# Kernel tuning notes

Hardware: AMD Instinct MI355X
Metric: run time of the kernel (lower is better)

## Reference

```python
import jax, jax.numpy as jnp
import numpy as np

N_WIRES = 4
DIM = 2 ** N_WIRES  # 16 amplitudes per 4-qubit state
# PauliZ sign table: wire 0 is the most-significant bit of the flattened index
_SIGNS = (1.0 - 2.0 * ((np.arange(DIM)[:, None] >> np.array([3, 2, 1, 0])[None, :]) & 1)).astype(np.float32)  # [16,4]


def _rx(state, theta, wire):
    """Apply RX(theta) on `wire`. state: [N,2,2,2,2] complex64; theta: [N] or scalar."""
    c = jnp.cos(theta / 2.0)
    s = -1j * jnp.sin(theta / 2.0)
    c = c.astype(jnp.complex64).reshape(c.shape + (1, 1, 1))
    s = s.astype(jnp.complex64).reshape(s.shape + (1, 1, 1))
    st = jnp.moveaxis(state, wire + 1, -1)
    a0, a1 = st[..., 0], st[..., 1]
    new = jnp.stack([c * a0 + s * a1, s * a0 + c * a1], axis=-1)
    return jnp.moveaxis(new, -1, wire + 1)


def _cnot(state, ctrl, tgt):
    s = jnp.moveaxis(state, (ctrl + 1, tgt + 1), (1, 2))
    s = jnp.stack([s[:, 0], s[:, 1, ::-1]], axis=1)
    return jnp.moveaxis(s, (1, 2), (ctrl + 1, tgt + 1))


def _simulate(angles, q_params):
    """angles: [N,4] RX encoding angles; q_params: [n_layers,4]. Returns PauliZ expvals [N,4]."""
    N = angles.shape[0]
    state = jnp.zeros((N, DIM), jnp.complex64).at[:, 0].set(1.0).reshape((N, 2, 2, 2, 2))
    for w in range(N_WIRES):                      # encoder: RX(x_w) on wire w
        state = _rx(state, angles[:, w], w)
    for l in range(q_params.shape[0]):            # variational layers
        for w in range(N_WIRES):
            state = _rx(state, q_params[l, w], w)
        for src in range(N_WIRES):                # CNOT ring (i, (i+1)%4)
            state = _cnot(state, src, (src + 1) % N_WIRES)
    probs = jnp.abs(state.reshape(N, DIM)) ** 2
    return probs @ jnp.asarray(_SIGNS)            # [N,4]


def setup_inputs() -> dict:
    key = jax.random.key(0)
    k1, k2, k3 = jax.random.split(key, 3)
    B, S, E = 8, 1024, 128
    x = jax.random.normal(k1, (B, S, E), dtype=jnp.float32)
    q_params = jax.random.normal(k2, (1, 4), dtype=jnp.float32)
    W_combine = jax.random.normal(k3, (E, E), dtype=jnp.float32) / jnp.sqrt(jnp.float32(E))
    return {"x": x, "q_params": q_params, "W_combine": W_combine}


def reference(x, q_params, W_combine):
    B, S, E = x.shape
    H, DK = 32, 4
    # quantum encoding of every (token, head) chunk -- q, k, v are identical
    angles = x.reshape(B * S * H, DK)
    qkv = _simulate(angles, q_params).reshape(B, S, H, DK)
    h = jnp.transpose(qkv, (0, 2, 1, 3))          # [B,H,S,DK]
    scores = jnp.einsum('bhqd,bhkd->bhqk', h, h) / jnp.sqrt(jnp.float32(DK))
    attn = jax.nn.softmax(scores, axis=-1)        # dropout is identity in eval
    out = jnp.einsum('bhqk,bhkd->bhqd', attn, h)
    out = jnp.transpose(out, (0, 2, 1, 3)).reshape(B, S, E)
    return out @ W_combine.T                      # combine_heads (no bias)
```

## Files before the change

kernel.cpp:

```cpp
#include <hip/hip_runtime.h>

constexpr int kS = 1024;
constexpr int NM = 126;

typedef __fp16 fp16x2 __attribute__((ext_vector_type(2)));
typedef _Float16 half4v __attribute__((ext_vector_type(4)));
typedef _Float16 half8v __attribute__((ext_vector_type(8)));
typedef float float4v __attribute__((ext_vector_type(4)));


__device__ __forceinline__ float wcoef(int a0, int a1, int a2, int a3) {
  const float b[6] = {1.0031455f, 1.0010453f, 0.4860342f,
                      0.1641117f, 0.0507286f, 0.0097257f};
  const float f[6] = {1.f, 1.f, 2.f, 6.f, 24.f, 120.f};
  const float p2[6] = {1.f, 2.f, 4.f, 8.f, 16.f, 32.f};
  int n = a0 + a1 + a2 + a3;
  return b[n] * f[n] / (p2[n] * f[a0] * f[a1] * f[a2] * f[a3]);
}

template <class F>
__device__ __forceinline__ void for_each_mono(float z0, float z1, float z2,
                                              float z3, F&& f) {
  int idx = 0;
  float p0 = 1.f;
#pragma unroll
  for (int a0 = 0; a0 <= 5; ++a0) {
    float p1 = p0;
#pragma unroll
    for (int a1 = 0; a1 <= 5 - a0; ++a1) {
      float p2 = p1;
#pragma unroll
      for (int a2 = 0; a2 <= 5 - a0 - a1; ++a2) {
        float p3 = p2;
#pragma unroll
        for (int a3 = 0; a3 <= 5 - a0 - a1 - a2; ++a3) {
          f(idx, p3, a0, a1, a2, a3);
          ++idx;
          p3 *= z3;
        }
        p2 *= z2;
      }
      p1 *= z1;
    }
    p0 *= z0;
  }
}

__global__ __launch_bounds__(256) void qenc_kernel(
    const float4* __restrict__ x4, const float* __restrict__ qp,
    uint2* __restrict__ h16u) {
  int idx = blockIdx.x * 256 + threadIdx.x;
  float4 a = x4[idx];
  float c0 = cosf(a.x + qp[0]);
  float c1 = cosf(a.y + qp[1]);
  float c2 = cosf(a.z + qp[2]);
  float c3 = cosf(a.w + qp[3]);
  float z1 = c0 * c1;
  float z2 = z1 * c2;
  float z3 = z2 * c3;
  float z0 = c1 * c2 * c3;
  union { half4v h; uint2 u; } z;
  z.h.x = (_Float16)z0;
  z.h.y = (_Float16)z1;
  z.h.z = (_Float16)z2;
  z.h.w = (_Float16)z3;
  int b = idx >> 15;
  int s = (idx >> 5) & (kS - 1);
  int head = idx & 31;
  int bh = b * 32 + head;
  h16u[(bh << 10) + s] = z.u;
}

__global__ __launch_bounds__(256) void featM_kernel(
    const _Float16* __restrict__ h16, float* __restrict__ Mpart) {
  __shared__ ushort sm[128][136];
  __shared__ ushort vvb[2048];
  const int bh = blockIdx.x >> 1;
  const int half = blockIdx.x & 1;
  const int t = threadIdx.x;
  const bool hiH = t >= 128;
  const int tok = t & 127;
  const uint2* __restrict__ hb = (const uint2*)(h16) + (bh << 10) + (half << 9);

  for (int i = t; i < 2 * 136; i += 256) sm[126 + i / 136][i % 136] = 0;
  for (int i = t; i < 2048; i += 256)
    vvb[i] = (((i >> 3) & 15) == 4) ? (ushort)0x3C00u : (ushort)0u;

  const int lane = t & 63;
  const int w = t >> 6;
  const int c = lane & 15, g = lane >> 4;
  float4v acc[2] = {};

  for (int ch = 0; ch < 4; ++ch) {
    __syncthreads();
    {
      union { uint2 u; half4v h; ushort4 us; } uz;
      uz.u = hb[(ch << 7) + tok];
      float z0 = (float)uz.h.x, z1 = (float)uz.h.y;
      float z2 = (float)uz.h.z, z3 = (float)uz.h.w;
      if (!hiH) {
        int base = ((tok >> 3) << 7) + (tok & 7);
        vvb[base + 0] = uz.us.x;
        vvb[base + 8] = uz.us.y;
        vvb[base + 16] = uz.us.z;
        vvb[base + 24] = uz.us.w;
      }
      for_each_mono(z0, z1, z2, z3,
                    [&](int mi, float m, int, int, int, int) {
                      if (hiH ? (mi >= 63) : (mi < 63)) {
                        union { _Float16 h; ushort u; } cv;
                        cv.h = (_Float16)m;
                        sm[mi][tok] = cv.u;
                      }
                    });
    }
    __syncthreads();
    {
      const uint4* __restrict__ vvb4 = (const uint4*)vvb;
      union U4H { uint4 u; half8v h; };
#pragma unroll
      for (int ks = 0; ks < 4; ++ks) {
        U4H ub;
        ub.u = vvb4[(((ks << 2) + g) << 4) + c];
#pragma unroll
        for (int tl = 0; tl < 2; ++tl) {
          const uint4* arow4 = (const uint4*)&sm[(w << 5) + (tl << 4) + c][0];
          U4H ua;
          ua.u = arow4[(ks << 2) + g];
          acc[tl] = __builtin_amdgcn_mfma_f32_16x16x32_f16(ua.h, ub.h,
                                                           acc[tl], 0, 0, 0);
        }
      }
    }
  }

  if (c < 5) {
    float* mp = Mpart + ((bh << 1) + half) * NM * 5;
#pragma unroll
    for (int tl = 0; tl < 2; ++tl) {
#pragma unroll
      for (int reg = 0; reg < 4; ++reg) {
        int row = (w << 5) + (tl << 4) + (g << 2) + reg;
        if (row < NM) mp[row * 5 + c] = acc[tl][reg];
      }
    }
  }
}

__global__ __launch_bounds__(256) void featC_kernel(
    const _Float16* __restrict__ h16, const float* __restrict__ Mpart,
    uint2* __restrict__ o16u2) {
  __shared__ float Mw[NM][8];
  const int bh = blockIdx.x >> 2;
  const int qc = blockIdx.x & 3;
  const int t = threadIdx.x;
  if (t < NM) {
    const float* m0 = Mpart + ((bh << 1) * NM + t) * 5;
    const float* m1 = m0 + NM * 5;
#pragma unroll
    for (int c = 0; c < 5; ++c) Mw[t][c] = m0[c] + m1[c];
  }
  __syncthreads();

  const int q = (qc << 8) + t;
  union { uint2 u; half4v h; } uz;
  uz.u = ((const uint2*)h16)[(bh << 10) + q];
  float z0 = (float)uz.h.x, z1 = (float)uz.h.y;
  float z2 = (float)uz.h.z, z3 = (float)uz.h.w;

  float n0 = 0.f, n1 = 0.f, n2 = 0.f, n3 = 0.f, den = 0.f;
  for_each_mono(z0, z1, z2, z3,
                [&](int mi, float m, int a0, int a1, int a2, int a3) {
                  float wm = m * wcoef(a0, a1, a2, a3);
                  float4 M4 = *(const float4*)&Mw[mi][0];
                  n0 += wm * M4.x; n1 += wm * M4.y;
                  n2 += wm * M4.z; n3 += wm * M4.w;
                  den += wm * Mw[mi][4];
                });

  float inv = 1.0f / den;
  union { fp16x2 p[2]; uint2 u; } res;
  res.p[0] = __builtin_amdgcn_cvt_pkrtz(n0 * inv, n1 * inv);
  res.p[1] = __builtin_amdgcn_cvt_pkrtz(n2 * inv, n3 * inv);
  int b = bh >> 5, head = bh & 31;
  o16u2[(((b << 10) + q) << 5) + head] = res.u;
}

__global__ __launch_bounds__(256) void wtb_kernel(
    const float* __restrict__ W, _Float16* __restrict__ wtb) {
  int i = blockIdx.x * 256 + threadIdx.x;
  int col = i >> 7, e = i & 127;
  wtb[((e >> 3) << 10) + (col << 3) + (e & 7)] = (_Float16)W[i];
}

__global__ __launch_bounds__(256) void combine_kernel(
    const _Float16* __restrict__ o16, const _Float16* __restrict__ wtb,
    float* __restrict__ out) {
  const int lane = threadIdx.x & 63;
  const int wv = threadIdx.x >> 6;
  const int job = blockIdx.x * 4 + wv;
  const int rt = job >> 3, ct = job & 7;
  const int c = lane & 15, g = lane >> 4;
  const uint4* a4 = (const uint4*)o16;
  const uint4* b4 = (const uint4*)wtb;
  const int arow = (rt << 4) + c;
  union U4H { uint4 u; half8v h; };
  float4v acc = {};
#pragma unroll
  for (int t = 0; t < 4; ++t) {
    U4H ua, ub;
    ua.u = a4[(arow << 4) + (t << 2) + g];
    ub.u = b4[(((t << 2) + g) << 7) + (ct << 4) + c];
    acc = __builtin_amdgcn_mfma_f32_16x16x32_f16(ua.h, ub.h, acc, 0, 0, 0);
  }
  const int orow = (rt << 4) + (g << 2);
  const int ocol = (ct << 4) + c;
#pragma unroll
  for (int reg = 0; reg < 4; ++reg)
    out[(orow + reg) * 128 + ocol] = acc[reg];
}

extern "C" void kernel_launch(void* const* d_in, const int* in_sizes, int n_in,
                              void* d_out, int out_size, void* d_ws,
                              size_t ws_size, hipStream_t stream) {
  const float* x = (const float*)d_in[0];
  const float* qp = (const float*)d_in[1];
  const float* W = (const float*)d_in[2];
  float* out = (float*)d_out;

  char* ws = (char*)d_ws;
  _Float16* h16 = (_Float16*)ws;
  float* Mpart = (float*)(ws + (2 << 20));
  _Float16* o16 = (_Float16*)(ws + (6 << 20));
  _Float16* wtb = (_Float16*)(ws + (8 << 20));

  wtb_kernel<<<64, 256, 0, stream>>>(W, wtb);
  qenc_kernel<<<1024, 256, 0, stream>>>((const float4*)x, qp, (uint2*)h16);
  featM_kernel<<<512, 256, 0, stream>>>(h16, Mpart);
  featC_kernel<<<1024, 256, 0, stream>>>(h16, Mpart, (uint2*)o16);
  combine_kernel<<<1024, 256, 0, stream>>>(o16, wtb, out);
}
```

Before: 35.25 us.

## Move featC contraction to MFMA and fuse weight transpose into qenc

The per-query feature contraction in featC is now an fp16 MFMA product. It multiplies a shared-memory monomial matrix (128 queries by 126 monomials) by a coefficient-weighted M matrix, replacing the scalar 126-term loop per thread. Results are gathered with lane shuffles for the normalisation, and the grid doubles to 2048 blocks of 128 queries. Separately, the W transpose/cast kernel is folded into the first 64 blocks of qenc to drop one launch. The risk is lost precision, since the weighted M is now rounded to fp16, and shuffle work is added per output.

```diff
diff --git a/kernel.cpp b/kernel.cpp
--- a/kernel.cpp
+++ b/kernel.cpp
@@ -48,8 +48,14 @@
 
 __global__ __launch_bounds__(256) void qenc_kernel(
     const float4* __restrict__ x4, const float* __restrict__ qp,
-    uint2* __restrict__ h16u) {
+    uint2* __restrict__ h16u, const float* __restrict__ W,
+    _Float16* __restrict__ wtb) {
   int idx = blockIdx.x * 256 + threadIdx.x;
+  if (blockIdx.x < 64) {
+    int i = idx;
+    int col = i >> 7, e = i & 127;
+    wtb[((e >> 3) << 10) + (col << 3) + (e & 7)] = (_Float16)W[i];
+  }
   float4 a = x4[idx];
   float c0 = cosf(a.x + qp[0]);
   float c1 = cosf(a.y + qp[1]);
@@ -150,47 +156,102 @@
 __global__ __launch_bounds__(256) void featC_kernel(
     const _Float16* __restrict__ h16, const float* __restrict__ Mpart,
     uint2* __restrict__ o16u2) {
-  __shared__ float Mw[NM][8];
-  const int bh = blockIdx.x >> 2;
-  const int qc = blockIdx.x & 3;
+  __shared__ uint4 sm4[128][17];
+  __shared__ ushort mwb[2048];
+  const int bh = blockIdx.x >> 3;
+  const int qc = blockIdx.x & 7;
   const int t = threadIdx.x;
+
+  {
+    uint* mw32 = (uint*)mwb;
+    mw32[t] = 0u;
+    mw32[t + 256] = 0u;
+    mw32[t + 512] = 0u;
+    mw32[t + 768] = 0u;
+  }
+  __syncthreads();
+
   if (t < NM) {
-    const float* m0 = Mpart + ((bh << 1) * NM + t) * 5;
-    const float* m1 = m0 + NM * 5;
-#pragma unroll
-    for (int c = 0; c < 5; ++c) Mw[t][c] = m0[c] + m1[c];
+    float w = 0.f;
+    for_each_mono(1.f, 1.f, 1.f, 1.f,
+                  [&](int mi, float, int a0, int a1, int a2, int a3) {
+                    if (mi == t) w = wcoef(a0, a1, a2, a3);
+                  });
+    const float* p0 = Mpart + ((bh << 1) * NM + t) * 5;
+    const float* p1 = p0 + NM * 5;
+    int base = ((t >> 3) << 7) + (t & 7);
+#pragma unroll
+    for (int c = 0; c < 5; ++c) {
+      union { _Float16 h; ushort u; } cv;
+      cv.h = (_Float16)(w * (p0[c] + p1[c]));
+      mwb[base + (c << 3)] = cv.u;
+    }
+  }
+
+  {
+    const int row = t & 127;
+    const bool hiH = t >= 128;
+    union { uint2 u; half4v h; } uz;
+    uz.u = ((const uint2*)h16)[(bh << 10) + (qc << 7) + row];
+    float z0 = (float)uz.h.x, z1 = (float)uz.h.y;
+    float z2 = (float)uz.h.z, z3 = (float)uz.h.w;
+    ushort* srow = (ushort*)&sm4[row][0];
+    for_each_mono(z0, z1, z2, z3,
+                  [&](int mi, float m, int, int, int, int) {
+                    if (hiH ? (mi >= 63) : (mi < 63)) {
+                      union { _Float16 h; ushort u; } cv;
+                      cv.h = (_Float16)m;
+                      srow[mi] = cv.u;
+                    }
+                  });
+    if (hiH) {
+      uint* srow32 = (uint*)srow;
+      srow32[63] = 0u; srow32[64] = 0u; srow32[65] = 0u;
+      srow32[66] = 0u; srow32[67] = 0u;
+    }
   }
   __syncthreads();
 
-  const int q = (qc << 8) + t;
-  union { uint2 u; half4v h; } uz;
-  uz.u = ((const uint2*)h16)[(bh << 10) + q];
-  float z0 = (float)uz.h.x, z1 = (float)uz.h.y;
-  float z2 = (float)uz.h.z, z3 = (float)uz.h.w;
-
-  float n0 = 0.f, n1 = 0.f, n2 = 0.f, n3 = 0.f, den = 0.f;
-  for_each_mono(z0, z1, z2, z3,
-                [&](int mi, float m, int a0, int a1, int a2, int a3) {
-                  float wm = m * wcoef(a0, a1, a2, a3);
-                  float4 M4 = *(const float4*)&Mw[mi][0];
-                  n0 += wm * M4.x; n1 += wm * M4.y;
-                  n2 += wm * M4.z; n3 += wm * M4.w;
-                  den += wm * Mw[mi][4];
-                });
-
-  float inv = 1.0f / den;
-  union { fp16x2 p[2]; uint2 u; } res;
-  res.p[0] = __builtin_amdgcn_cvt_pkrtz(n0 * inv, n1 * inv);
-  res.p[1] = __builtin_amdgcn_cvt_pkrtz(n2 * inv, n3 * inv);
-  int b = bh >> 5, head = bh & 31;
-  o16u2[(((b << 10) + q) << 5) + head] = res.u;
-}
-
-__global__ __launch_bounds__(256) void wtb_kernel(
-    const float* __restrict__ W, _Float16* __restrict__ wtb) {
-  int i = blockIdx.x * 256 + threadIdx.x;
-  int col = i >> 7, e = i & 127;
-  wtb[((e >> 3) << 10) + (col << 3) + (e & 7)] = (_Float16)W[i];
+  const int lane = t & 63;
+  const int w_ = t >> 6;
+  const int c = lane & 15, g = lane >> 4;
+  const uint4* __restrict__ mwb4 = (const uint4*)mwb;
+  union U4H { uint4 u; half8v h; };
+  float4v acc[2] = {};
+#pragma unroll
+  for (int ks = 0; ks < 4; ++ks) {
+    U4H ub;
+    ub.u = mwb4[(((ks << 2) + g) << 4) + c];
+#pragma unroll
+    for (int tl = 0; tl < 2; ++tl) {
+      U4H ua;
+      ua.u = sm4[(w_ << 5) + (tl << 4) + c][(ks << 2) + g];
+      acc[tl] = __builtin_amdgcn_mfma_f32_16x16x32_f16(ua.h, ub.h,
+                                                       acc[tl], 0, 0, 0);
+    }
+  }
+
+  const int b_ = bh >> 5, head = bh & 31;
+  const int gbase = lane & 48;
+#pragma unroll
+  for (int tl = 0; tl < 2; ++tl) {
+#pragma unroll
+    for (int reg = 0; reg < 4; ++reg) {
+      float v = acc[tl][reg];
+      float n1 = __shfl(v, gbase | 1);
+      float n2 = __shfl(v, gbase | 2);
+      float n3 = __shfl(v, gbase | 3);
+      float den = __shfl(v, gbase | 4);
+      if (c == 0) {
+        float inv = 1.0f / den;
+        union { fp16x2 p[2]; uint2 u; } res;
+        res.p[0] = __builtin_amdgcn_cvt_pkrtz(v * inv, n1 * inv);
+        res.p[1] = __builtin_amdgcn_cvt_pkrtz(n2 * inv, n3 * inv);
+        int q = (qc << 7) + (w_ << 5) + (tl << 4) + (g << 2) + reg;
+        o16u2[(((b_ << 10) + q) << 5) + head] = res.u;
+      }
+    }
+  }
 }
 
 __global__ __launch_bounds__(256) void combine_kernel(
@@ -234,9 +295,9 @@
   _Float16* o16 = (_Float16*)(ws + (6 << 20));
   _Float16* wtb = (_Float16*)(ws + (8 << 20));
 
-  wtb_kernel<<<64, 256, 0, stream>>>(W, wtb);
-  qenc_kernel<<<1024, 256, 0, stream>>>((const float4*)x, qp, (uint2*)h16);
+  qenc_kernel<<<1024, 256, 0, stream>>>((const float4*)x, qp, (uint2*)h16, W,
+                                        wtb);
   featM_kernel<<<512, 256, 0, stream>>>(h16, Mpart);
-  featC_kernel<<<1024, 256, 0, stream>>>(h16, Mpart, (uint2*)o16);
+  featC_kernel<<<2048, 256, 0, stream>>>(h16, Mpart, (uint2*)o16);
   combine_kernel<<<1024, 256, 0, stream>>>(o16, wtb, out);
 }
```

New measurement: 41.73 us. 18.4% more time.
